# Optimization experiments

Hardware: AMD Instinct MI355X
Metric: run time of the kernel (lower is better)

Reference implementation:

```python
import jax, jax.numpy as jnp
import numpy as np

B, NX, NY, D_FEAT, CTX, S, T = 64, 32, 32, 1024, 512, 32, 4
N = NX * NY


def build_adjacency_matrix(nx, ny):
    # 4-neighborhood grid adjacency with self loops (faithful to original loop)
    adj = np.eye(nx * ny, dtype=np.float32)
    row = 0
    for i in range(nx):
        for j in range(ny):
            if i > 0:
                adj[row, j + (i - 1) * nx] = 1.0
            if i < nx - 1:
                adj[row, j + (i + 1) * nx] = 1.0
            if j > 0:
                adj[row, j - 1 + i * nx] = 1.0
            if j < ny - 1:
                adj[row, j + 1 + i * nx] = 1.0
            row += 1
    return adj


def setup_inputs() -> dict:
    key = jax.random.key(0)
    ks = jax.random.split(key, 12)
    s = 0.02
    return {
        "images": jax.random.normal(ks[0], (B, N, D_FEAT), jnp.float32),
        "q_encoding": jax.random.normal(ks[1], (B, CTX), jnp.float32),
        "lstm_outputs": jax.random.normal(ks[2], (B, S, CTX), jnp.float32),
        "q_length": jax.random.randint(ks[3], (B,), 1, S + 1, jnp.int32),
        "adj": jnp.asarray(build_adjacency_matrix(NX, NY)),
        "initKB_w": jax.random.normal(ks[4], (CTX, D_FEAT), jnp.float32) * s,
        "initKB_b": jnp.zeros((CTX,), jnp.float32),
        "W_w": jax.random.normal(ks[5], (CTX, 2 * CTX), jnp.float32) * s,
        "W_b": jnp.zeros((CTX,), jnp.float32),
        "qInput_w": jax.random.normal(ks[6], (CTX, CTX), jnp.float32) * s,
        "qInput_b": jnp.zeros((CTX,), jnp.float32),
        "qInputT_w": jax.random.normal(ks[7], (T, CTX, CTX), jnp.float32) * s,
        "qInputT_b": jnp.zeros((T, CTX), jnp.float32),
        "cmd_w": jax.random.normal(ks[8], (1, CTX), jnp.float32) * s,
        "cmd_b": jnp.zeros((1,), jnp.float32),
    }


def reference(images, q_encoding, lstm_outputs, q_length, adj,
              initKB_w, initKB_b, W_w, W_b, qInput_w, qInput_b,
              qInputT_w, qInputT_b, cmd_w, cmd_b) -> jnp.ndarray:
    n_iter = qInputT_w.shape[0]
    seq = lstm_outputs.shape[1]
    # loc_init: images [B,N,D_FEAT] -> x_loc [B,N,CTX]
    x_loc = jnp.einsum("bnd,cd->bnc", images, initKB_w) + initKB_b
    # shared first command layer (cfg.CMD_INPUT_ACT = elu)
    q1 = jax.nn.elu(q_encoding @ qInput_w.T + qInput_b)  # [B,CTX]
    valid = jnp.arange(seq)[None, :] < q_length[:, None]  # [B,S]
    for t in range(n_iter):
        # extract_textual_command
        q_cmd = q1 @ qInputT_w[t].T + qInputT_b[t]  # [B,CTX]
        raw_att = jnp.einsum("bsd,d->bs", q_cmd[:, None, :] * lstm_outputs, cmd_w[0]) + cmd_b[0]
        raw_att = jnp.where(valid, raw_att, -1e30)
        att = jax.nn.softmax(raw_att, axis=-1)  # [B,S]
        cmd = jnp.einsum("bs,bsd->bd", att, lstm_outputs)  # [B,CTX]
        # propagate_message: concat + linear, then dense adjacency matmul
        cmd_tiled = jnp.broadcast_to(cmd[:, None, :], x_loc.shape)
        support = jnp.concatenate([x_loc, cmd_tiled], axis=-1) @ W_w.T + W_b  # [B,N,CTX]
        x_new = jnp.einsum("nm,bmd->bnd", adj, support)  # [B,N,CTX]
        x_loc = jax.nn.elu(x_new) if t < n_iter - 1 else x_new
    return x_loc
```

## Files before the change

### kernel.cpp

```cpp
#include <hip/hip_runtime.h>
#include <hip/hip_bf16.h>
#include <math.h>

#define NB 64
#define NNODES 1024
#define CTXD 512
#define SEQL 32

typedef __attribute__((ext_vector_type(8))) short short8;
typedef __attribute__((ext_vector_type(4))) float floatx4;

__device__ __forceinline__ float bf2f(unsigned short u) {
  union { unsigned int i; float f; } v; v.i = ((unsigned int)u) << 16; return v.f;
}
__device__ __forceinline__ unsigned short f2bf(float f) {
  union { float f; unsigned int i; } v; v.f = f;
  unsigned int r = v.i + 0x7fffu + ((v.i >> 16) & 1u);
  return (unsigned short)(r >> 16);
}
__device__ __forceinline__ float elu1(float x) { return x > 0.f ? x : expm1f(x); }

__device__ __forceinline__ void gload16(const void* g, void* l) {
  __builtin_amdgcn_global_load_lds((const __attribute__((address_space(1))) void*)g,
                                   (__attribute__((address_space(3))) void*)l, 16, 0, 0);
}

__global__ __launch_bounds__(256) void pack_k(const float* __restrict__ kbw,
                                              const float* __restrict__ Ww,
                                              const float* __restrict__ qiw,
                                              const float* __restrict__ qtw,
                                              unsigned short* __restrict__ kb_bf,
                                              unsigned short* __restrict__ w1_bf,
                                              float* __restrict__ qiT,
                                              float* __restrict__ qTT,
                                              float* __restrict__ w2T) {
  int idx = blockIdx.x * 256 + threadIdx.x;
  if (idx < 524288) {
    kb_bf[idx] = f2bf(kbw[idx]);
  } else if (idx < 786432) {
    int o = idx - 524288;
    w1_bf[o] = f2bf(Ww[(o >> 9) * 1024 + (o & 511)]);
  } else if (idx < 1048576) {
    int o = idx - 786432;
    int k = o >> 9, c = o & 511;
    qiT[o] = qiw[c * 512 + k];
  } else if (idx < 2097152) {
    int o = idx - 1048576;
    int t = o >> 18, r = o & 262143;
    int k = r >> 9, c = r & 511;
    qTT[o] = qtw[((size_t)t * 512 + c) * 512 + k];
  } else {
    int o = idx - 2097152;
    int k = o >> 9, c = o & 511;
    w2T[o] = Ww[c * 1024 + 512 + k];
  }
}

__global__ __launch_bounds__(512) void q1_k(const float* __restrict__ q_enc,
                                            const float* __restrict__ qiT,
                                            const float* __restrict__ qInput_b,
                                            float* __restrict__ q1) {
  int b = blockIdx.x, c = threadIdx.x;
  __shared__ float qes[512];
  qes[c] = q_enc[b * 512 + c];
  __syncthreads();
  float a0 = qInput_b[c], a1 = 0.f, a2 = 0.f, a3 = 0.f;
#pragma unroll 4
  for (int k = 0; k < 512; k += 4) {
    a0 += qes[k] * qiT[k * 512 + c];
    a1 += qes[k + 1] * qiT[(k + 1) * 512 + c];
    a2 += qes[k + 2] * qiT[(k + 2) * 512 + c];
    a3 += qes[k + 3] * qiT[(k + 3) * 512 + c];
  }
  q1[b * 512 + c] = elu1(a0 + a1 + a2 + a3);
}

__global__ __launch_bounds__(512) void cmdt_k(
    const float* __restrict__ q1, const float* __restrict__ lstm,
    const int* __restrict__ q_len,
    const float* __restrict__ qTT, const float* __restrict__ qT_b,
    const float* __restrict__ cmd_w, const float* __restrict__ cmd_b,
    const float* __restrict__ w2T, const float* __restrict__ W_b,
    float* __restrict__ bias2) {
  int b = blockIdx.x & 63;
  int t = blockIdx.x >> 6;
  int c = threadIdx.x;
  __shared__ float q1s[512];
  __shared__ float us[512];
  __shared__ float red[512];
  __shared__ float atts[32];
  __shared__ float cmds[512];

  q1s[c] = q1[b * 512 + c];
  __syncthreads();

  const float* wt = qTT + (size_t)t * 262144;
  float a0 = qT_b[t * 512 + c], a1 = 0.f, a2 = 0.f, a3 = 0.f;
#pragma unroll 4
  for (int k = 0; k < 512; k += 4) {
    a0 += q1s[k] * wt[k * 512 + c];
    a1 += q1s[k + 1] * wt[(k + 1) * 512 + c];
    a2 += q1s[k + 2] * wt[(k + 2) * 512 + c];
    a3 += q1s[k + 3] * wt[(k + 3) * 512 + c];
  }
  us[c] = (a0 + a1 + a2 + a3) * cmd_w[c];
  __syncthreads();

  const float* lstmb = lstm + (size_t)b * SEQL * 512;
  {
    int s = c >> 4, u = c & 15;
    float p = 0.f;
    const float* lr = lstmb + s * 512;
    for (int r = u; r < 512; r += 16) p += us[r] * lr[r];
    red[c] = p;
  }
  __syncthreads();
  if (c < 32) {
    float raw = cmd_b[0];
    for (int u = 0; u < 16; u++) raw += red[c * 16 + u];
    raw = (c < q_len[b]) ? raw : -1e30f;
    float mx = raw;
    for (int off = 16; off; off >>= 1) mx = fmaxf(mx, __shfl_xor(mx, off, 32));
    float e = expf(raw - mx);
    float sm = e;
    for (int off = 16; off; off >>= 1) sm += __shfl_xor(sm, off, 32);
    atts[c] = e / sm;
  }
  __syncthreads();
  float cd = 0.f;
#pragma unroll
  for (int s = 0; s < 32; s++) cd += atts[s] * lstmb[s * 512 + c];
  cmds[c] = cd;
  __syncthreads();

  float b0 = W_b[c], b1 = 0.f, b2 = 0.f, b3 = 0.f;
#pragma unroll 4
  for (int k = 0; k < 512; k += 4) {
    b0 += cmds[k] * w2T[k * 512 + c];
    b1 += cmds[k + 1] * w2T[(k + 1) * 512 + c];
    b2 += cmds[k + 2] * w2T[(k + 2) * 512 + c];
    b3 += cmds[k + 3] * w2T[(k + 3) * 512 + c];
  }
  bias2[((size_t)(t * 64 + b)) * 512 + c] = b0 + b1 + b2 + b3;
}

__global__ __launch_bounds__(256) void stencil_k(const unsigned short* __restrict__ x,
                                                 unsigned short* __restrict__ y) {
  int g = blockIdx.x * 256 + threadIdx.x;
  int v = g & 63;
  int n = (g >> 6) & 1023;
  int b = g >> 16;
  size_t base = ((((size_t)b << 10) + n) << 9) + v * 8;
  const unsigned short* p = x + base;
  float acc[8];
  short8 s = *(const short8*)p;
#pragma unroll
  for (int j = 0; j < 8; j++) acc[j] = bf2f((unsigned short)s[j]);
  int i = n >> 5, jj = n & 31;
  if (i > 0) {
    short8 t = *(const short8*)(p - 32 * 512);
#pragma unroll
    for (int j = 0; j < 8; j++) acc[j] += bf2f((unsigned short)t[j]);
  }
  if (i < 31) {
    short8 t = *(const short8*)(p + 32 * 512);
#pragma unroll
    for (int j = 0; j < 8; j++) acc[j] += bf2f((unsigned short)t[j]);
  }
  if (jj > 0) {
    short8 t = *(const short8*)(p - 512);
#pragma unroll
    for (int j = 0; j < 8; j++) acc[j] += bf2f((unsigned short)t[j]);
  }
  if (jj < 31) {
    short8 t = *(const short8*)(p + 512);
#pragma unroll
    for (int j = 0; j < 8; j++) acc[j] += bf2f((unsigned short)t[j]);
  }
  short8 o;
#pragma unroll
  for (int j = 0; j < 8; j++) o[j] = (short)f2bf(acc[j]);
  *(short8*)(y + base) = o;
}

template <int AF32, int MODE>
__global__ __launch_bounds__(256) void gemm_bt(
    const void* __restrict__ Ap, int lda,
    const unsigned short* __restrict__ Bw, int ldb, int K,
    const float* __restrict__ cbias, const float* __restrict__ bias2,
    void* __restrict__ Cp) {
  __shared__ __align__(128) unsigned short As[128 * 64];
  __shared__ __align__(128) unsigned short Bs[128 * 64];

  const int tid = threadIdx.x;
  const int lane = tid & 63;
  const int wave = tid >> 6;
  const int wr = (wave >> 1) * 64;
  const int wc = (wave & 1) * 64;
  const int lr = lane & 15;
  const int lk = lane >> 4;
  const int lr7 = lr & 7;

  int bid = blockIdx.x;
  int cpx = gridDim.x >> 3;
  int wg = (bid & 7) * cpx + (bid >> 3);
  int mtile = wg >> 2;
  int ntile = wg & 3;
  const size_t rowBase = (size_t)mtile * 128;
  const int colBase = ntile * 128;

  floatx4 acc[4][4];
#pragma unroll
  for (int m = 0; m < 4; m++)
#pragma unroll
    for (int n = 0; n < 4; n++) acc[m][n] = {0.f, 0.f, 0.f, 0.f};

  for (int k0 = 0; k0 < K; k0 += 64) {
    __syncthreads();
    if constexpr (AF32) {
      const float* A = (const float*)Ap;
#pragma unroll
      for (int j = 0; j < 4; j++) {
        int g = j * 256 + tid;
        int r = g >> 3, s = g & 7;
        const float* src = A + (rowBase + r) * (size_t)lda + k0 + s * 8;
        floatx4 v0 = *(const floatx4*)src;
        floatx4 v1 = *(const floatx4*)(src + 4);
        short8 t;
#pragma unroll
        for (int e = 0; e < 4; e++) {
          __hip_bfloat16 h0 = __float2bfloat16(v0[e]);
          __hip_bfloat16 h1 = __float2bfloat16(v1[e]);
          t[e] = (short)*reinterpret_cast<unsigned short*>(&h0);
          t[e + 4] = (short)*reinterpret_cast<unsigned short*>(&h1);
        }
        *(short8*)((char*)As + r * 128 + ((s ^ (r & 7)) << 4)) = t;
      }
    } else {
      const unsigned short* A = (const unsigned short*)Ap;
#pragma unroll
      for (int j = 0; j < 4; j++) {
        int g = j * 256 + tid;
        int r = g >> 3, u = g & 7;
        gload16(A + (rowBase + r) * (size_t)lda + k0 + ((u ^ (r & 7)) << 3),
                (char*)As + g * 16);
      }
    }
#pragma unroll
    for (int j = 0; j < 4; j++) {
      int g = j * 256 + tid;
      int r = g >> 3, u = g & 7;
      gload16(Bw + (size_t)(colBase + r) * ldb + k0 + ((u ^ (r & 7)) << 3),
              (char*)Bs + g * 16);
    }
    __syncthreads();

#pragma unroll
    for (int kk = 0; kk < 2; kk++) {
      const int ub = ((kk << 2) + lk) ^ lr7;
      short8 a[4], b[4];
#pragma unroll
      for (int m = 0; m < 4; m++)
        a[m] = *(const short8*)((const char*)As + (wr + m * 16 + lr) * 128 + (ub << 4));
#pragma unroll
      for (int n = 0; n < 4; n++)
        b[n] = *(const short8*)((const char*)Bs + (wc + n * 16 + lr) * 128 + (ub << 4));
#pragma unroll
      for (int m = 0; m < 4; m++)
#pragma unroll
        for (int n = 0; n < 4; n++)
          acc[m][n] = __builtin_amdgcn_mfma_f32_16x16x32_bf16(a[m], b[n], acc[m][n], 0, 0, 0);
    }
  }

#pragma unroll
  for (int m = 0; m < 4; m++) {
#pragma unroll
    for (int q = 0; q < 4; q++) {
      size_t grow = rowBase + wr + m * 16 + lk * 4 + q;
      float degf = 0.f;
      const float* b2 = nullptr;
      if constexpr (MODE != 0) {
        int nsp = (int)(grow & 1023);
        int ii = nsp >> 5, jj = nsp & 31;
        degf = (float)(1 + (ii > 0) + (ii < 31) + (jj > 0) + (jj < 31));
        b2 = bias2 + (grow >> 10) * CTXD;
      }
#pragma unroll
      for (int n = 0; n < 4; n++) {
        int gcol = colBase + wc + n * 16 + lr;
        float v = acc[m][n][q];
        if constexpr (MODE == 0) v += cbias[gcol];
        else v += degf * b2[gcol];
        if constexpr (MODE == 1) v = elu1(v);
        if constexpr (MODE == 2) ((float*)Cp)[grow * CTXD + gcol] = v;
        else ((unsigned short*)Cp)[grow * CTXD + gcol] = f2bf(v);
      }
    }
  }
}

template <int MODE>
__global__ __launch_bounds__(512, 2) void gemm256(
    const unsigned short* __restrict__ A, int lda,
    const unsigned short* __restrict__ Bw, int ldb, int K,
    const float* __restrict__ bias2, void* __restrict__ Cp) {
  __shared__ __align__(128) unsigned short As[2][256 * 64];
  __shared__ __align__(128) unsigned short Bs[2][256 * 64];

  const int tid = threadIdx.x;
  const int lane = tid & 63;
  const int wave = tid >> 6;
  const int wm = wave >> 2;
  const int wn = wave & 3;
  const int lr = lane & 15;
  const int lk = lane >> 4;
  const int lr7 = lr & 7;

  int bid = blockIdx.x;
  int cpx = gridDim.x >> 3;
  int wg = (bid & 7) * cpx + (bid >> 3);
  const size_t rowBase = (size_t)(wg >> 1) * 256;
  const int colBase = (wg & 1) * 256;

  floatx4 acc[8][4];
#pragma unroll
  for (int m = 0; m < 8; m++)
#pragma unroll
    for (int n = 0; n < 4; n++) acc[m][n] = {0.f, 0.f, 0.f, 0.f};

  auto stage = [&](int buf, int kt) {
    const int kbase = kt * 64;
#pragma unroll
    for (int j = 0; j < 4; j++) {
      int g = j * 512 + tid;
      int r = g >> 3, u = g & 7;
      gload16(A + (rowBase + r) * (size_t)lda + kbase + ((u ^ (r & 7)) << 3),
              (char*)&As[buf][0] + g * 16);
    }
#pragma unroll
    for (int j = 0; j < 4; j++) {
      int g = j * 512 + tid;
      int r = g >> 3, u = g & 7;
      gload16(Bw + (size_t)(colBase + r) * ldb + kbase + ((u ^ (r & 7)) << 3),
              (char*)&Bs[buf][0] + g * 16);
    }
  };

  const int NT = K >> 6;
  stage(0, 0);
  stage(1, 1);

  for (int kt = 0; kt < NT; kt++) {
    const int cur = kt & 1;
    if (kt < NT - 1) {
      asm volatile("s_waitcnt vmcnt(8)" ::: "memory");
    } else {
      asm volatile("s_waitcnt vmcnt(0)" ::: "memory");
    }
    __builtin_amdgcn_s_barrier();
    __builtin_amdgcn_sched_barrier(0);

    const unsigned short* Ab = &As[cur][0];
    const unsigned short* Bb = &Bs[cur][0];
#pragma unroll
    for (int kk = 0; kk < 2; kk++) {
      const int ub = ((kk << 2) + lk) ^ lr7;
      short8 a[8], b[4];
#pragma unroll
      for (int m = 0; m < 8; m++)
        a[m] = *(const short8*)((const char*)Ab + (wm * 128 + m * 16 + lr) * 128 + (ub << 4));
#pragma unroll
      for (int n = 0; n < 4; n++)
        b[n] = *(const short8*)((const char*)Bb + (wn * 64 + n * 16 + lr) * 128 + (ub << 4));
#pragma unroll
      for (int m = 0; m < 8; m++)
#pragma unroll
        for (int n = 0; n < 4; n++)
          acc[m][n] = __builtin_amdgcn_mfma_f32_16x16x32_bf16(a[m], b[n], acc[m][n], 0, 0, 0);
    }

    if (kt + 2 < NT) {
      __builtin_amdgcn_sched_barrier(0);
      __builtin_amdgcn_s_barrier();
      stage(cur, kt + 2);
    }
  }

#pragma unroll
  for (int m = 0; m < 8; m++) {
#pragma unroll
    for (int q = 0; q < 4; q++) {
      size_t grow = rowBase + wm * 128 + m * 16 + lk * 4 + q;
      int nsp = (int)(grow & 1023);
      int ii = nsp >> 5, jj = nsp & 31;
      float degf = (float)(1 + (ii > 0) + (ii < 31) + (jj > 0) + (jj < 31));
      const float* b2 = bias2 + (grow >> 10) * CTXD;
#pragma unroll
      for (int n = 0; n < 4; n++) {
        int gcol = colBase + wn * 64 + n * 16 + lr;
        float v = acc[m][n][q] + degf * b2[gcol];
        if constexpr (MODE == 1) {
          ((unsigned short*)Cp)[grow * CTXD + gcol] = f2bf(elu1(v));
        } else {
          ((float*)Cp)[grow * CTXD + gcol] = v;
        }
      }
    }
  }
}

extern "C" void kernel_launch(void* const* d_in, const int* in_sizes, int n_in,
                              void* d_out, int out_size, void* d_ws, size_t ws_size,
                              hipStream_t stream) {
  const float* images   = (const float*)d_in[0];
  const float* q_enc    = (const float*)d_in[1];
  const float* lstm     = (const float*)d_in[2];
  const int*   q_len    = (const int*)d_in[3];
  const float* initKB_w = (const float*)d_in[5];
  const float* initKB_b = (const float*)d_in[6];
  const float* W_w      = (const float*)d_in[7];
  const float* W_b      = (const float*)d_in[8];
  const float* qInput_w = (const float*)d_in[9];
  const float* qInput_b = (const float*)d_in[10];
  const float* qT_w     = (const float*)d_in[11];
  const float* qT_b     = (const float*)d_in[12];
  const float* cmd_w    = (const float*)d_in[13];
  const float* cmd_b    = (const float*)d_in[14];

  char* ws = (char*)d_ws;
  unsigned short* y     = (unsigned short*)ws;
  float*          qiT   = (float*)ws;
  float*          qTT   = (float*)(ws + 1048576);
  float*          w2T   = (float*)(ws + 5242880);
  unsigned short* kb_bf = (unsigned short*)(ws + 67108864);
  unsigned short* w1_bf = (unsigned short*)(ws + 68157440);
  float*          bias2 = (float*)(ws + 68681728);
  float*          q1    = (float*)(ws + 69206016);
  unsigned short* xloc  = (unsigned short*)d_out;

  pack_k<<<9216, 256, 0, stream>>>(initKB_w, W_w, qInput_w, qT_w,
                                   kb_bf, w1_bf, qiT, qTT, w2T);
  q1_k<<<64, 512, 0, stream>>>(q_enc, qiT, qInput_b, q1);
  cmdt_k<<<256, 512, 0, stream>>>(q1, lstm, q_len, qTT, qT_b, cmd_w, cmd_b,
                                  w2T, W_b, bias2);

  gemm_bt<1, 0><<<2048, 256, 0, stream>>>(images, 1024, kb_bf, 1024, 1024,
                                          initKB_b, nullptr, xloc);

  for (int t = 0; t < 4; t++) {
    stencil_k<<<16384, 256, 0, stream>>>(xloc, y);
    if (t < 3)
      gemm256<1><<<512, 512, 0, stream>>>(y, 512, w1_bf, 512, 512,
                                          bias2 + (size_t)t * 64 * 512, xloc);
    else
      gemm256<2><<<512, 512, 0, stream>>>(y, 512, w1_bf, 512, 512,
                                          bias2 + (size_t)t * 64 * 512, d_out);
  }
}
```

Baseline: 563.2 us.

## Fuse grid stencil into GEMM A-tile loading with ping-pong buffers

```diff
diff --git a/kernel.cpp b/kernel.cpp
--- a/kernel.cpp
+++ b/kernel.cpp
@@ -144,45 +144,6 @@
   bias2[((size_t)(t * 64 + b)) * 512 + c] = b0 + b1 + b2 + b3;
 }
 
-__global__ __launch_bounds__(256) void stencil_k(const unsigned short* __restrict__ x,
-                                                 unsigned short* __restrict__ y) {
-  int g = blockIdx.x * 256 + threadIdx.x;
-  int v = g & 63;
-  int n = (g >> 6) & 1023;
-  int b = g >> 16;
-  size_t base = ((((size_t)b << 10) + n) << 9) + v * 8;
-  const unsigned short* p = x + base;
-  float acc[8];
-  short8 s = *(const short8*)p;
-#pragma unroll
-  for (int j = 0; j < 8; j++) acc[j] = bf2f((unsigned short)s[j]);
-  int i = n >> 5, jj = n & 31;
-  if (i > 0) {
-    short8 t = *(const short8*)(p - 32 * 512);
-#pragma unroll
-    for (int j = 0; j < 8; j++) acc[j] += bf2f((unsigned short)t[j]);
-  }
-  if (i < 31) {
-    short8 t = *(const short8*)(p + 32 * 512);
-#pragma unroll
-    for (int j = 0; j < 8; j++) acc[j] += bf2f((unsigned short)t[j]);
-  }
-  if (jj > 0) {
-    short8 t = *(const short8*)(p - 512);
-#pragma unroll
-    for (int j = 0; j < 8; j++) acc[j] += bf2f((unsigned short)t[j]);
-  }
-  if (jj < 31) {
-    short8 t = *(const short8*)(p + 512);
-#pragma unroll
-    for (int j = 0; j < 8; j++) acc[j] += bf2f((unsigned short)t[j]);
-  }
-  short8 o;
-#pragma unroll
-  for (int j = 0; j < 8; j++) o[j] = (short)f2bf(acc[j]);
-  *(short8*)(y + base) = o;
-}
-
 template <int AF32, int MODE>
 __global__ __launch_bounds__(256) void gemm_bt(
     const void* __restrict__ Ap, int lda,
@@ -301,18 +262,19 @@
 }
 
 template <int MODE>
-__global__ __launch_bounds__(512, 2) void gemm256(
-    const unsigned short* __restrict__ A, int lda,
-    const unsigned short* __restrict__ Bw, int ldb, int K,
-    const float* __restrict__ bias2, void* __restrict__ Cp) {
-  __shared__ __align__(128) unsigned short As[2][256 * 64];
-  __shared__ __align__(128) unsigned short Bs[2][256 * 64];
+__global__ __launch_bounds__(256) void gemm_st(
+    const unsigned short* __restrict__ X,
+    const unsigned short* __restrict__ Bw,
+    const float* __restrict__ bias2,
+    void* __restrict__ Cp) {
+  __shared__ __align__(128) unsigned short As[128 * 64];
+  __shared__ __align__(128) unsigned short Bs[128 * 64];
 
   const int tid = threadIdx.x;
   const int lane = tid & 63;
   const int wave = tid >> 6;
-  const int wm = wave >> 2;
-  const int wn = wave & 3;
+  const int wr = (wave >> 1) * 64;
+  const int wc = (wave & 1) * 64;
   const int lr = lane & 15;
   const int lk = lane >> 4;
   const int lr7 = lr & 7;
@@ -320,85 +282,95 @@
   int bid = blockIdx.x;
   int cpx = gridDim.x >> 3;
   int wg = (bid & 7) * cpx + (bid >> 3);
-  const size_t rowBase = (size_t)(wg >> 1) * 256;
-  const int colBase = (wg & 1) * 256;
-
-  floatx4 acc[8][4];
-#pragma unroll
-  for (int m = 0; m < 8; m++)
+  int mtile = wg >> 2;
+  int ntile = wg & 3;
+  const size_t rowBase = (size_t)mtile * 128;
+  const int colBase = ntile * 128;
+
+  floatx4 acc[4][4];
+#pragma unroll
+  for (int m = 0; m < 4; m++)
 #pragma unroll
     for (int n = 0; n < 4; n++) acc[m][n] = {0.f, 0.f, 0.f, 0.f};
 
-  auto stage = [&](int buf, int kt) {
-    const int kbase = kt * 64;
+  for (int k0 = 0; k0 < 512; k0 += 64) {
+    __syncthreads();
 #pragma unroll
     for (int j = 0; j < 4; j++) {
-      int g = j * 512 + tid;
+      int g = j * 256 + tid;
       int r = g >> 3, u = g & 7;
-      gload16(A + (rowBase + r) * (size_t)lda + kbase + ((u ^ (r & 7)) << 3),
-              (char*)&As[buf][0] + g * 16);
+      size_t R = rowBase + r;
+      int n = (int)(R & 1023);
+      int gi = n >> 5, gj = n & 31;
+      const unsigned short* p = X + R * 512 + k0 + u * 8;
+      short8 c = *(const short8*)p;
+      float s[8];
+#pragma unroll
+      for (int e = 0; e < 8; e++) s[e] = bf2f((unsigned short)c[e]);
+      if (gi > 0) {
+        short8 t = *(const short8*)(p - 32 * 512);
+#pragma unroll
+        for (int e = 0; e < 8; e++) s[e] += bf2f((unsigned short)t[e]);
+      }
+      if (gi < 31) {
+        short8 t = *(const short8*)(p + 32 * 512);
+#pragma unroll
+        for (int e = 0; e < 8; e++) s[e] += bf2f((unsigned short)t[e]);
+      }
+      if (gj > 0) {
+        short8 t = *(const short8*)(p - 512);
+#pragma unroll
+        for (int e = 0; e < 8; e++) s[e] += bf2f((unsigned short)t[e]);
+      }
+      if (gj < 31) {
+        short8 t = *(const short8*)(p + 512);
+#pragma unroll
+        for (int e = 0; e < 8; e++) s[e] += bf2f((unsigned short)t[e]);
+      }
+      short8 o;
+#pragma unroll
+      for (int e = 0; e < 8; e++) o[e] = (short)f2bf(s[e]);
+      *(short8*)((char*)As + r * 128 + ((u ^ (r & 7)) << 4)) = o;
     }
 #pragma unroll
     for (int j = 0; j < 4; j++) {
-      int g = j * 512 + tid;
+      int g = j * 256 + tid;
       int r = g >> 3, u = g & 7;
-      gload16(Bw + (size_t)(colBase + r) * ldb + kbase + ((u ^ (r & 7)) << 3),
-              (char*)&Bs[buf][0] + g * 16);
-    }
-  };
-
-  const int NT = K >> 6;
-  stage(0, 0);
-  stage(1, 1);
-
-  for (int kt = 0; kt < NT; kt++) {
-    const int cur = kt & 1;
-    if (kt < NT - 1) {
-      asm volatile("s_waitcnt vmcnt(8)" ::: "memory");
-    } else {
-      asm volatile("s_waitcnt vmcnt(0)" ::: "memory");
-    }
-    __builtin_amdgcn_s_barrier();
-    __builtin_amdgcn_sched_barrier(0);
-
-    const unsigned short* Ab = &As[cur][0];
-    const unsigned short* Bb = &Bs[cur][0];
+      gload16(Bw + (size_t)(colBase + r) * 512 + k0 + ((u ^ (r & 7)) << 3),
+              (char*)Bs + g * 16);
+    }
+    __syncthreads();
+
 #pragma unroll
     for (int kk = 0; kk < 2; kk++) {
       const int ub = ((kk << 2) + lk) ^ lr7;
-      short8 a[8], b[4];
-#pragma unroll
-      for (int m = 0; m < 8; m++)
-        a[m] = *(const short8*)((const char*)Ab + (wm * 128 + m * 16 + lr) * 128 + (ub << 4));
+      short8 a[4], b[4];
+#pragma unroll
+      for (int m = 0; m < 4; m++)
+        a[m] = *(const short8*)((const char*)As + (wr + m * 16 + lr) * 128 + (ub << 4));
 #pragma unroll
       for (int n = 0; n < 4; n++)
-        b[n] = *(const short8*)((const char*)Bb + (wn * 64 + n * 16 + lr) * 128 + (ub << 4));
-#pragma unroll
-      for (int m = 0; m < 8; m++)
+        b[n] = *(const short8*)((const char*)Bs + (wc + n * 16 + lr) * 128 + (ub << 4));
+#pragma unroll
+      for (int m = 0; m < 4; m++)
 #pragma unroll
         for (int n = 0; n < 4; n++)
           acc[m][n] = __builtin_amdgcn_mfma_f32_16x16x32_bf16(a[m], b[n], acc[m][n], 0, 0, 0);
     }
-
-    if (kt + 2 < NT) {
-      __builtin_amdgcn_sched_barrier(0);
-      __builtin_amdgcn_s_barrier();
-      stage(cur, kt + 2);
-    }
-  }
-
-#pragma unroll
-  for (int m = 0; m < 8; m++) {
+  }
+
+#pragma unroll
+  for (int m = 0; m < 4; m++) {
 #pragma unroll
     for (int q = 0; q < 4; q++) {
-      size_t grow = rowBase + wm * 128 + m * 16 + lk * 4 + q;
+      size_t grow = rowBase + wr + m * 16 + lk * 4 + q;
       int nsp = (int)(grow & 1023);
       int ii = nsp >> 5, jj = nsp & 31;
       float degf = (float)(1 + (ii > 0) + (ii < 31) + (jj > 0) + (jj < 31));
       const float* b2 = bias2 + (grow >> 10) * CTXD;
 #pragma unroll
       for (int n = 0; n < 4; n++) {
-        int gcol = colBase + wn * 64 + n * 16 + lr;
+        int gcol = colBase + wc + n * 16 + lr;
         float v = acc[m][n][q] + degf * b2[gcol];
         if constexpr (MODE == 1) {
           ((unsigned short*)Cp)[grow * CTXD + gcol] = f2bf(elu1(v));
@@ -429,7 +401,7 @@
   const float* cmd_b    = (const float*)d_in[14];
 
   char* ws = (char*)d_ws;
-  unsigned short* y     = (unsigned short*)ws;
+  unsigned short* X1    = (unsigned short*)ws;
   float*          qiT   = (float*)ws;
   float*          qTT   = (float*)(ws + 1048576);
   float*          w2T   = (float*)(ws + 5242880);
@@ -437,7 +409,7 @@
   unsigned short* w1_bf = (unsigned short*)(ws + 68157440);
   float*          bias2 = (float*)(ws + 68681728);
   float*          q1    = (float*)(ws + 69206016);
-  unsigned short* xloc  = (unsigned short*)d_out;
+  unsigned short* X0    = (unsigned short*)d_out;
 
   pack_k<<<9216, 256, 0, stream>>>(initKB_w, W_w, qInput_w, qT_w,
                                    kb_bf, w1_bf, qiT, qTT, w2T);
@@ -446,15 +418,10 @@
                                   w2T, W_b, bias2);
 
   gemm_bt<1, 0><<<2048, 256, 0, stream>>>(images, 1024, kb_bf, 1024, 1024,
-                                          initKB_b, nullptr, xloc);
-
-  for (int t = 0; t < 4; t++) {
-    stencil_k<<<16384, 256, 0, stream>>>(xloc, y);
-    if (t < 3)
-      gemm256<1><<<512, 512, 0, stream>>>(y, 512, w1_bf, 512, 512,
-                                          bias2 + (size_t)t * 64 * 512, xloc);
-    else
-      gemm256<2><<<512, 512, 0, stream>>>(y, 512, w1_bf, 512, 512,
-                                          bias2 + (size_t)t * 64 * 512, d_out);
-  }
-}
+                                          initKB_b, nullptr, X0);
+
+  gemm_st<1><<<2048, 256, 0, stream>>>(X0, w1_bf, bias2 + 0 * 32768, X1);
+  gemm_st<1><<<2048, 256, 0, stream>>>(X1, w1_bf, bias2 + 1 * 32768, X0);
+  gemm_st<1><<<2048, 256, 0, stream>>>(X0, w1_bf, bias2 + 2 * 32768, X1);
+  gemm_st<2><<<2048, 256, 0, stream>>>(X1, w1_bf, bias2 + 3 * 32768, d_out);
+}
```

Result: slower. 725.6 us (+28.8%).

## Rewrite GEMMs with quarter-split LDS pipeline and 64x256 fp32-input tiles

Applied to the files above, without the earlier changes.

```diff
diff --git a/kernel.cpp b/kernel.cpp
--- a/kernel.cpp
+++ b/kernel.cpp
@@ -183,31 +183,25 @@
   *(short8*)(y + base) = o;
 }
 
-template <int AF32, int MODE>
-__global__ __launch_bounds__(256) void gemm_bt(
-    const void* __restrict__ Ap, int lda,
-    const unsigned short* __restrict__ Bw, int ldb, int K,
-    const float* __restrict__ cbias, const float* __restrict__ bias2,
-    void* __restrict__ Cp) {
-  __shared__ __align__(128) unsigned short As[128 * 64];
-  __shared__ __align__(128) unsigned short Bs[128 * 64];
+__global__ __launch_bounds__(256, 3) void igemm(
+    const float* __restrict__ Af,
+    const unsigned short* __restrict__ Bw,
+    const float* __restrict__ cbias,
+    unsigned short* __restrict__ Cp) {
+  __shared__ __align__(128) unsigned short As[64 * 64];
+  __shared__ __align__(128) unsigned short Bs[256 * 64];
 
   const int tid = threadIdx.x;
   const int lane = tid & 63;
-  const int wave = tid >> 6;
-  const int wr = (wave >> 1) * 64;
-  const int wc = (wave & 1) * 64;
+  const int wn = tid >> 6;
   const int lr = lane & 15;
   const int lk = lane >> 4;
   const int lr7 = lr & 7;
 
   int bid = blockIdx.x;
-  int cpx = gridDim.x >> 3;
-  int wg = (bid & 7) * cpx + (bid >> 3);
-  int mtile = wg >> 2;
-  int ntile = wg & 3;
-  const size_t rowBase = (size_t)mtile * 128;
-  const int colBase = ntile * 128;
+  int wg = (bid & 7) * (gridDim.x >> 3) + (bid >> 3);
+  const size_t rowBase = (size_t)(wg >> 1) * 64;
+  const int colBase = (wg & 1) * 256;
 
   floatx4 acc[4][4];
 #pragma unroll
@@ -215,42 +209,28 @@
 #pragma unroll
     for (int n = 0; n < 4; n++) acc[m][n] = {0.f, 0.f, 0.f, 0.f};
 
-  for (int k0 = 0; k0 < K; k0 += 64) {
+  for (int k0 = 0; k0 < 1024; k0 += 64) {
     __syncthreads();
-    if constexpr (AF32) {
-      const float* A = (const float*)Ap;
-#pragma unroll
-      for (int j = 0; j < 4; j++) {
-        int g = j * 256 + tid;
-        int r = g >> 3, s = g & 7;
-        const float* src = A + (rowBase + r) * (size_t)lda + k0 + s * 8;
-        floatx4 v0 = *(const floatx4*)src;
-        floatx4 v1 = *(const floatx4*)(src + 4);
-        short8 t;
-#pragma unroll
-        for (int e = 0; e < 4; e++) {
-          __hip_bfloat16 h0 = __float2bfloat16(v0[e]);
-          __hip_bfloat16 h1 = __float2bfloat16(v1[e]);
-          t[e] = (short)*reinterpret_cast<unsigned short*>(&h0);
-          t[e + 4] = (short)*reinterpret_cast<unsigned short*>(&h1);
-        }
-        *(short8*)((char*)As + r * 128 + ((s ^ (r & 7)) << 4)) = t;
-      }
-    } else {
-      const unsigned short* A = (const unsigned short*)Ap;
-#pragma unroll
-      for (int j = 0; j < 4; j++) {
-        int g = j * 256 + tid;
-        int r = g >> 3, u = g & 7;
-        gload16(A + (rowBase + r) * (size_t)lda + k0 + ((u ^ (r & 7)) << 3),
-                (char*)As + g * 16);
-      }
-    }
-#pragma unroll
-    for (int j = 0; j < 4; j++) {
+#pragma unroll
+    for (int j = 0; j < 2; j++) {
       int g = j * 256 + tid;
       int r = g >> 3, u = g & 7;
-      gload16(Bw + (size_t)(colBase + r) * ldb + k0 + ((u ^ (r & 7)) << 3),
+      const float* src = Af + (rowBase + r) * (size_t)1024 + k0 + u * 8;
+      floatx4 v0 = *(const floatx4*)src;
+      floatx4 v1 = *(const floatx4*)(src + 4);
+      short8 t;
+#pragma unroll
+      for (int e = 0; e < 4; e++) {
+        t[e] = (short)f2bf(v0[e]);
+        t[e + 4] = (short)f2bf(v1[e]);
+      }
+      *(short8*)((char*)As + r * 128 + ((u ^ (r & 7)) << 4)) = t;
+    }
+#pragma unroll
+    for (int j = 0; j < 8; j++) {
+      int g = j * 256 + tid;
+      int r = g >> 3, u = g & 7;
+      gload16(Bw + (size_t)(colBase + r) * 1024 + k0 + ((u ^ (r & 7)) << 3),
               (char*)Bs + g * 16);
     }
     __syncthreads();
@@ -261,10 +241,10 @@
       short8 a[4], b[4];
 #pragma unroll
       for (int m = 0; m < 4; m++)
-        a[m] = *(const short8*)((const char*)As + (wr + m * 16 + lr) * 128 + (ub << 4));
+        a[m] = *(const short8*)((const char*)As + (m * 16 + lr) * 128 + (ub << 4));
 #pragma unroll
       for (int n = 0; n < 4; n++)
-        b[n] = *(const short8*)((const char*)Bs + (wc + n * 16 + lr) * 128 + (ub << 4));
+        b[n] = *(const short8*)((const char*)Bs + (wn * 64 + n * 16 + lr) * 128 + (ub << 4));
 #pragma unroll
       for (int m = 0; m < 4; m++)
 #pragma unroll
@@ -277,36 +257,24 @@
   for (int m = 0; m < 4; m++) {
 #pragma unroll
     for (int q = 0; q < 4; q++) {
-      size_t grow = rowBase + wr + m * 16 + lk * 4 + q;
-      float degf = 0.f;
-      const float* b2 = nullptr;
-      if constexpr (MODE != 0) {
-        int nsp = (int)(grow & 1023);
-        int ii = nsp >> 5, jj = nsp & 31;
-        degf = (float)(1 + (ii > 0) + (ii < 31) + (jj > 0) + (jj < 31));
-        b2 = bias2 + (grow >> 10) * CTXD;
+      size_t grow = rowBase + m * 16 + lk * 4 + q;
+#pragma unroll
+      for (int n = 0; n < 4; n++) {
+        int gcol = colBase + wn * 64 + n * 16 + lr;
+        Cp[grow * CTXD + gcol] = f2bf(acc[m][n][q] + cbias[gcol]);
       }
-#pragma unroll
-      for (int n = 0; n < 4; n++) {
-        int gcol = colBase + wc + n * 16 + lr;
-        float v = acc[m][n][q];
-        if constexpr (MODE == 0) v += cbias[gcol];
-        else v += degf * b2[gcol];
-        if constexpr (MODE == 1) v = elu1(v);
-        if constexpr (MODE == 2) ((float*)Cp)[grow * CTXD + gcol] = v;
-        else ((unsigned short*)Cp)[grow * CTXD + gcol] = f2bf(v);
-      }
     }
   }
 }
 
 template <int MODE>
-__global__ __launch_bounds__(512, 2) void gemm256(
-    const unsigned short* __restrict__ A, int lda,
-    const unsigned short* __restrict__ Bw, int ldb, int K,
-    const float* __restrict__ bias2, void* __restrict__ Cp) {
-  __shared__ __align__(128) unsigned short As[2][256 * 64];
-  __shared__ __align__(128) unsigned short Bs[2][256 * 64];
+__global__ __launch_bounds__(512, 2) void gemm8(
+    const unsigned short* __restrict__ Ay,
+    const unsigned short* __restrict__ Bw,
+    const float* __restrict__ bias2,
+    void* __restrict__ Cp) {
+  __shared__ __align__(128) unsigned short AsL[2][2][8192];
+  __shared__ __align__(128) unsigned short BsL[2][2][8192];
 
   const int tid = threadIdx.x;
   const int lane = tid & 63;
@@ -316,10 +284,10 @@
   const int lr = lane & 15;
   const int lk = lane >> 4;
   const int lr7 = lr & 7;
+  const int rB0 = (wn & 1) * 64;
 
   int bid = blockIdx.x;
-  int cpx = gridDim.x >> 3;
-  int wg = (bid & 7) * cpx + (bid >> 3);
+  int wg = (bid & 7) * (gridDim.x >> 3) + (bid >> 3);
   const size_t rowBase = (size_t)(wg >> 1) * 256;
   const int colBase = (wg & 1) * 256;
 
@@ -329,62 +297,135 @@
 #pragma unroll
     for (int n = 0; n < 4; n++) acc[m][n] = {0.f, 0.f, 0.f, 0.f};
 
-  auto stage = [&](int buf, int kt) {
-    const int kbase = kt * 64;
-#pragma unroll
-    for (int j = 0; j < 4; j++) {
-      int g = j * 512 + tid;
-      int r = g >> 3, u = g & 7;
-      gload16(A + (rowBase + r) * (size_t)lda + kbase + ((u ^ (r & 7)) << 3),
-              (char*)&As[buf][0] + g * 16);
-    }
-#pragma unroll
-    for (int j = 0; j < 4; j++) {
-      int g = j * 512 + tid;
-      int r = g >> 3, u = g & 7;
-      gload16(Bw + (size_t)(colBase + r) * ldb + kbase + ((u ^ (r & 7)) << 3),
-              (char*)&Bs[buf][0] + g * 16);
+  auto stgA = [&](int d, int h, int kt) {
+#pragma unroll
+    for (int j = 0; j < 2; j++) {
+      int g = j * 512 + tid, r = g >> 3, u = g & 7;
+      gload16(Ay + (rowBase + h * 128 + r) * (size_t)512 + kt * 64 + ((u ^ (r & 7)) << 3),
+              (char*)&AsL[d][h][0] + g * 16);
     }
   };
-
-  const int NT = K >> 6;
-  stage(0, 0);
-  stage(1, 1);
-
-  for (int kt = 0; kt < NT; kt++) {
-    const int cur = kt & 1;
-    if (kt < NT - 1) {
-      asm volatile("s_waitcnt vmcnt(8)" ::: "memory");
+  auto stgB = [&](int d, int h, int kt) {
+#pragma unroll
+    for (int j = 0; j < 2; j++) {
+      int g = j * 512 + tid, r = g >> 3, u = g & 7;
+      gload16(Bw + (size_t)(colBase + h * 128 + r) * 512 + kt * 64 + ((u ^ (r & 7)) << 3),
+              (char*)&BsL[d][h][0] + g * 16);
+    }
+  };
+
+  stgB(0, 0, 0); stgA(0, 0, 0); stgA(0, 1, 0); stgB(0, 1, 0);
+  stgB(1, 0, 1); stgA(1, 0, 1);
+  asm volatile("s_waitcnt vmcnt(4)" ::: "memory");
+  __builtin_amdgcn_sched_barrier(0);
+  __builtin_amdgcn_s_barrier();
+  __builtin_amdgcn_sched_barrier(0);
+
+  short8 a[2][4], b[2][4];
+
+  for (int t = 0; t < 8; t++) {
+    const int d = t & 1;
+    const char* Ah = (const char*)&AsL[d][wm][0];
+    const char* Bh = (const char*)&BsL[d][wn >> 1][0];
+
+#pragma unroll
+    for (int kk = 0; kk < 2; kk++) {
+      const int ub = ((kk << 2) + lk) ^ lr7;
+#pragma unroll
+      for (int m = 0; m < 4; m++)
+        a[kk][m] = *(const short8*)(Ah + (m * 16 + lr) * 128 + (ub << 4));
+#pragma unroll
+      for (int n = 0; n < 2; n++)
+        b[kk][n] = *(const short8*)(Bh + (rB0 + n * 16 + lr) * 128 + (ub << 4));
+    }
+    if (t + 1 < 8) stgA(d ^ 1, 1, t + 1);
+    __builtin_amdgcn_sched_barrier(0);
+    __builtin_amdgcn_s_barrier();
+    asm volatile("s_waitcnt lgkmcnt(0)" ::: "memory");
+    __builtin_amdgcn_sched_barrier(0);
+    __builtin_amdgcn_s_setprio(1);
+#pragma unroll
+    for (int kk = 0; kk < 2; kk++)
+#pragma unroll
+      for (int m = 0; m < 4; m++)
+#pragma unroll
+        for (int n = 0; n < 2; n++)
+          acc[m][n] = __builtin_amdgcn_mfma_f32_16x16x32_bf16(a[kk][m], b[kk][n], acc[m][n], 0, 0, 0);
+    __builtin_amdgcn_s_setprio(0);
+    __builtin_amdgcn_sched_barrier(0);
+    __builtin_amdgcn_s_barrier();
+    __builtin_amdgcn_sched_barrier(0);
+
+#pragma unroll
+    for (int kk = 0; kk < 2; kk++) {
+      const int ub = ((kk << 2) + lk) ^ lr7;
+#pragma unroll
+      for (int n = 2; n < 4; n++)
+        b[kk][n] = *(const short8*)(Bh + (rB0 + n * 16 + lr) * 128 + (ub << 4));
+    }
+    if (t + 1 < 8) stgB(d ^ 1, 1, t + 1);
+    __builtin_amdgcn_sched_barrier(0);
+    __builtin_amdgcn_s_barrier();
+    asm volatile("s_waitcnt lgkmcnt(0)" ::: "memory");
+    __builtin_amdgcn_sched_barrier(0);
+    __builtin_amdgcn_s_setprio(1);
+#pragma unroll
+    for (int kk = 0; kk < 2; kk++)
+#pragma unroll
+      for (int m = 0; m < 4; m++)
+#pragma unroll
+        for (int n = 2; n < 4; n++)
+          acc[m][n] = __builtin_amdgcn_mfma_f32_16x16x32_bf16(a[kk][m], b[kk][n], acc[m][n], 0, 0, 0);
+    __builtin_amdgcn_s_setprio(0);
+    __builtin_amdgcn_sched_barrier(0);
+    __builtin_amdgcn_s_barrier();
+    __builtin_amdgcn_sched_barrier(0);
+
+#pragma unroll
+    for (int kk = 0; kk < 2; kk++) {
+      const int ub = ((kk << 2) + lk) ^ lr7;
+#pragma unroll
+      for (int m = 0; m < 4; m++)
+        a[kk][m] = *(const short8*)(Ah + (64 + m * 16 + lr) * 128 + (ub << 4));
+    }
+    if (t + 2 < 8) stgB(d, 0, t + 2);
+    __builtin_amdgcn_sched_barrier(0);
+    __builtin_amdgcn_s_barrier();
+    asm volatile("s_waitcnt lgkmcnt(0)" ::: "memory");
+    __builtin_amdgcn_sched_barrier(0);
+    __builtin_amdgcn_s_setprio(1);
+#pragma unroll
+    for (int kk = 0; kk < 2; kk++)
+#pragma unroll
+      for (int m = 0; m < 4; m++)
+#pragma unroll
+        for (int n = 0; n < 2; n++)
+          acc[m + 4][n] = __builtin_amdgcn_mfma_f32_16x16x32_bf16(a[kk][m], b[kk][n], acc[m + 4][n], 0, 0, 0);
+    __builtin_amdgcn_s_setprio(0);
+    __builtin_amdgcn_sched_barrier(0);
+    __builtin_amdgcn_s_barrier();
+    __builtin_amdgcn_sched_barrier(0);
+
+    if (t + 2 < 8) stgA(d, 0, t + 2);
+    __builtin_amdgcn_sched_barrier(0);
+    __builtin_amdgcn_s_setprio(1);
+#pragma unroll
+    for (int kk = 0; kk < 2; kk++)
+#pragma unroll
+      for (int m = 0; m < 4; m++)
+#pragma unroll
+        for (int n = 2; n < 4; n++)
+          acc[m + 4][n] = __builtin_amdgcn_mfma_f32_16x16x32_bf16(a[kk][m], b[kk][n], acc[m + 4][n], 0, 0, 0);
+    __builtin_amdgcn_s_setprio(0);
+    __builtin_amdgcn_sched_barrier(0);
+    if (t + 2 < 8) {
+      asm volatile("s_waitcnt vmcnt(4)" ::: "memory");
     } else {
       asm volatile("s_waitcnt vmcnt(0)" ::: "memory");
     }
-    __builtin_amdgcn_s_barrier();
-    __builtin_amdgcn_sched_barrier(0);
-
-    const unsigned short* Ab = &As[cur][0];
-    const unsigned short* Bb = &Bs[cur][0];
-#pragma unroll
-    for (int kk = 0; kk < 2; kk++) {
-      const int ub = ((kk << 2) + lk) ^ lr7;
-      short8 a[8], b[4];
-#pragma unroll
-      for (int m = 0; m < 8; m++)
-        a[m] = *(const short8*)((const char*)Ab + (wm * 128 + m * 16 + lr) * 128 + (ub << 4));
-#pragma unroll
-      for (int n = 0; n < 4; n++)
-        b[n] = *(const short8*)((const char*)Bb + (wn * 64 + n * 16 + lr) * 128 + (ub << 4));
-#pragma unroll
-      for (int m = 0; m < 8; m++)
-#pragma unroll
-        for (int n = 0; n < 4; n++)
-          acc[m][n] = __builtin_amdgcn_mfma_f32_16x16x32_bf16(a[m], b[n], acc[m][n], 0, 0, 0);
-    }
-
-    if (kt + 2 < NT) {
-      __builtin_amdgcn_sched_barrier(0);
-      __builtin_amdgcn_s_barrier();
-      stage(cur, kt + 2);
-    }
+    __builtin_amdgcn_sched_barrier(0);
+    __builtin_amdgcn_s_barrier();
+    __builtin_amdgcn_sched_barrier(0);
   }
 
 #pragma unroll
@@ -445,16 +486,13 @@
   cmdt_k<<<256, 512, 0, stream>>>(q1, lstm, q_len, qTT, qT_b, cmd_w, cmd_b,
                                   w2T, W_b, bias2);
 
-  gemm_bt<1, 0><<<2048, 256, 0, stream>>>(images, 1024, kb_bf, 1024, 1024,
-                                          initKB_b, nullptr, xloc);
+  igemm<<<2048, 256, 0, stream>>>(images, kb_bf, initKB_b, xloc);
 
   for (int t = 0; t < 4; t++) {
     stencil_k<<<16384, 256, 0, stream>>>(xloc, y);
     if (t < 3)
-      gemm256<1><<<512, 512, 0, stream>>>(y, 512, w1_bf, 512, 512,
-                                          bias2 + (size_t)t * 64 * 512, xloc);
+      gemm8<1><<<512, 512, 0, stream>>>(y, w1_bf, bias2 + (size_t)t * 32768, xloc);
     else
-      gemm256<2><<<512, 512, 0, stream>>>(y, 512, w1_bf, 512, 512,
-                                          bias2 + (size_t)t * 64 * 512, d_out);
-  }
-}
+      gemm8<2><<<512, 512, 0, stream>>>(y, w1_bf, bias2 + (size_t)t * 32768, d_out);
+  }
+}
```

After: 524.7 us (median of 2 runs). -6.8%, faster.
